# Kernel tuning notes

Measured on AMD Instinct MI355X. Metric: run time of the kernel, lower is better.

The kernel has to match this reference:

```python
import jax, jax.numpy as jnp
import numpy as np

C = 64
CQ = C // 8


def setup_inputs() -> dict:
    key = jax.random.key(0)
    ks = jax.random.split(key, 8)
    scale = 0.05
    x = jax.random.normal(ks[0], (4, C, 64, 64), dtype=jnp.float32)
    Wq = jax.random.normal(ks[1], (CQ, C), dtype=jnp.float32) * scale
    bq = jax.random.normal(ks[2], (CQ,), dtype=jnp.float32) * scale
    Wk = jax.random.normal(ks[3], (CQ, C), dtype=jnp.float32) * scale
    bk = jax.random.normal(ks[4], (CQ,), dtype=jnp.float32) * scale
    Wv = jax.random.normal(ks[5], (C, C), dtype=jnp.float32) * scale
    bv = jax.random.normal(ks[6], (C,), dtype=jnp.float32) * scale
    gamma = jnp.zeros((1,), dtype=jnp.float32) + 0.5  # nonzero so output depends on attention
    return {"x": x, "Wq": Wq, "bq": bq, "Wk": Wk, "bk": bk, "Wv": Wv, "bv": bv, "gamma": gamma}


def reference(x, Wq, bq, Wk, bk, Wv, bv, gamma):
    bs, c, h, w = x.shape
    hw = h * w
    xf = x.reshape(bs, c, hw)  # [b, c, hw]
    # 1x1 convs == per-pixel linear over channels
    Q = jnp.einsum('oc,bcn->bon', Wq, xf) + bq[None, :, None]  # [b, c/8, hw]
    K = jnp.einsum('oc,bcn->bon', Wk, xf) + bk[None, :, None]  # [b, c/8, hw]
    V = jnp.einsum('oc,bcn->bon', Wv, xf) + bv[None, :, None]  # [b, c, hw]
    # attention = softmax(Q^T K, axis=-1), NO scaling (matches source)
    scores = jnp.einsum('bqn,bqm->bnm', Q, K)  # [b, hw, hw]
    attn = jax.nn.softmax(scores, axis=-1)
    out = jnp.einsum('bcm,bmn->bcn', V, attn)  # torch.bmm(V_, attention)
    out = out.reshape(bs, c, h, w)
    return gamma[0] * out + x
```

## Files before the change

kernel.cpp:

```cpp
#include <hip/hip_runtime.h>


constexpr int Bn = 4, Cc = 64, Q8 = 8, Np = 4096;
constexpr int QK_STR = 32;
constexpr int PSTR = 40;
constexpr int NSL = 4;
constexpr int KSTR = 40;

typedef float f32x4 __attribute__((ext_vector_type(4)));
typedef short short8 __attribute__((ext_vector_type(8)));

__device__ inline unsigned int f2bf(float x) {
    unsigned int u = __float_as_uint(x);
    u += 0x7fff + ((u >> 16) & 1);
    return u >> 16;
}
__device__ inline float bf2f(unsigned int u) { return __uint_as_float(u << 16); }

__device__ inline unsigned cvt_pk_bf16(float a, float b) {
    unsigned r;
    asm("v_cvt_pk_bf16_f32 %0, %1, %2" : "=v"(r) : "v"(a), "v"(b));
    return r;
}
__device__ inline float exp2g(float x) {
#if __has_builtin(__builtin_amdgcn_exp2f)
    return __builtin_amdgcn_exp2f(x);
#else
    return exp2f(x);
#endif
}
__device__ inline float log2g(float x) {
#if __has_builtin(__builtin_amdgcn_logf)
    return __builtin_amdgcn_logf(x);
#else
    return log2f(x);
#endif
}

__global__ __launch_bounds__(64) void qkv_v2(
    const float* __restrict__ x,
    const float* __restrict__ Wq, const float* __restrict__ bq,
    const float* __restrict__ Wk, const float* __restrict__ bk,
    const float* __restrict__ Wv, const float* __restrict__ bv,
    unsigned short* __restrict__ Qp, unsigned short* __restrict__ Kp,
    unsigned short* __restrict__ Vb)
{
    const int lane = threadIdx.x;
    const int gpos = blockIdx.x * 64;
    const int os = blockIdx.y;
    const int b = gpos >> 12, n = (gpos & (Np - 1)) + lane;
    const float LOG2E = 1.4426950408889634f;

    float xv[Cc];
    const float* xp = x + (size_t)(b * Cc) * Np + n;
    #pragma unroll
    for (int c = 0; c < Cc; c++) xv[c] = xp[(size_t)c * Np];

    if (os == 0) {
        unsigned pk[4];
        float a0, a1;
        #pragma unroll
        for (int p = 0; p < 4; p++) {
            a0 = bq[2 * p]; a1 = bq[2 * p + 1];
            #pragma unroll
            for (int c = 0; c < Cc; c++) {
                a0 += Wq[(2 * p) * Cc + c] * xv[c];
                a1 += Wq[(2 * p + 1) * Cc + c] * xv[c];
            }
            pk[p] = f2bf(a0 * LOG2E) | (f2bf(a1 * LOG2E) << 16);
        }
        unsigned short* qrow = Qp + (size_t)(b * Np + n) * QK_STR;
        *(uint4*)qrow = make_uint4(pk[0], pk[1], pk[2], pk[3]);
        *(uint4*)(qrow + 8)  = make_uint4(0, 0, 0, 0);
        *(uint4*)(qrow + 16) = make_uint4(0, 0, 0, 0);
        *(uint4*)(qrow + 24) = make_uint4(0, 0, 0, 0);
        #pragma unroll
        for (int p = 0; p < 4; p++) {
            a0 = bk[2 * p]; a1 = bk[2 * p + 1];
            #pragma unroll
            for (int c = 0; c < Cc; c++) {
                a0 += Wk[(2 * p) * Cc + c] * xv[c];
                a1 += Wk[(2 * p + 1) * Cc + c] * xv[c];
            }
            pk[p] = f2bf(a0) | (f2bf(a1) << 16);
        }
        unsigned short* krow = Kp + (size_t)(b * Np + n) * QK_STR;
        *(uint4*)krow = make_uint4(pk[0], pk[1], pk[2], pk[3]);
        *(uint4*)(krow + 8)  = make_uint4(0, 0, 0, 0);
        *(uint4*)(krow + 16) = make_uint4(0, 0, 0, 0);
        *(uint4*)(krow + 24) = make_uint4(0, 0, 0, 0);
        #pragma unroll
        for (int o = 0; o < 4; o++) {
            float a = bv[o];
            #pragma unroll
            for (int c = 0; c < Cc; c++) a += Wv[o * Cc + c] * xv[c];
            Vb[(size_t)(b * Cc + o) * Np + n] = (unsigned short)f2bf(a);
        }
    } else {
        const int vbase = os * 20 - 16;
        #pragma unroll 4
        for (int o = 0; o < 20; o++) {
            const int vr = vbase + o;
            float a = bv[vr];
            #pragma unroll
            for (int c = 0; c < Cc; c++) a += Wv[vr * Cc + c] * xv[c];
            Vb[(size_t)(b * Cc + vr) * Np + n] = (unsigned short)f2bf(a);
        }
    }
}

__global__ __launch_bounds__(256) void zsum_v2(
    const unsigned short* __restrict__ Qp, const unsigned short* __restrict__ Kp,
    float* __restrict__ ZP)
{
    __shared__ unsigned short Klds[64 * KSTR];
    const int tid = threadIdx.x, w = tid >> 6, lane = tid & 63;
    const int quad = lane >> 4, l15 = lane & 15;
    const int bz = blockIdx.z, ns = blockIdx.y;
    const int m0 = blockIdx.x * 64 + w * 16;

    short8 qa = *(const short8*)&Qp[((size_t)(bz * Np + m0 + l15)) * QK_STR + quad * 8];

    const int rt = tid >> 2, ct = tid & 3;
    const int nbase = ns * (Np / NSL);
    const unsigned short* kbase = Kp + (size_t)bz * Np * QK_STR;

    uint4 pf = *(const uint4*)&kbase[(size_t)(nbase + rt) * QK_STR + ct * 8];
    float z0 = 0.f, z1 = 0.f, z2 = 0.f, z3 = 0.f;
    for (int nt = 0; nt < Np / NSL; nt += 64) {
        *(uint4*)&Klds[rt * KSTR + ct * 8] = pf;
        __syncthreads();
        if (nt + 64 < Np / NSL)
            pf = *(const uint4*)&kbase[(size_t)(nbase + nt + 64 + rt) * QK_STR + ct * 8];
        #pragma unroll
        for (int t16 = 0; t16 < 4; t16++) {
            short8 kb = *(const short8*)&Klds[(t16 * 16 + l15) * KSTR + quad * 8];
            f32x4 s = __builtin_amdgcn_mfma_f32_16x16x32_bf16(
                qa, kb, f32x4{0.f, 0.f, 0.f, 0.f}, 0, 0, 0);
            z0 += exp2g(s[0]); z1 += exp2g(s[1]);
            z2 += exp2g(s[2]); z3 += exp2g(s[3]);
        }
        __syncthreads();
    }
    #pragma unroll
    for (int mask = 1; mask < 16; mask <<= 1) {
        z0 += __shfl_xor(z0, mask); z1 += __shfl_xor(z1, mask);
        z2 += __shfl_xor(z2, mask); z3 += __shfl_xor(z3, mask);
    }
    if (l15 == 0) {
        float4 v = make_float4(z0, z1, z2, z3);
        *(float4*)&ZP[((size_t)(bz * NSL + ns)) * Np + m0 + quad * 4] = v;
    }
}

__global__ __launch_bounds__(256) void zred(
    const float* __restrict__ ZP, float* __restrict__ Lg)
{
    int i = blockIdx.x * 256 + threadIdx.x;
    int b = i >> 12, m = i & (Np - 1);
    float z = 0.f;
    #pragma unroll
    for (int s = 0; s < NSL; s++) z += ZP[((size_t)(b * NSL + s)) * Np + m];
    Lg[(size_t)b * Np + m] = -log2g(z);
}

__global__ __launch_bounds__(256) void attn_v4(
    const unsigned short* __restrict__ Qp, const unsigned short* __restrict__ Kp,
    const unsigned short* __restrict__ Vb, const float* __restrict__ Lg,
    unsigned short* __restrict__ PO, int Ms, int SL)
{
    __shared__ unsigned short Plds[128 * PSTR];
    const int tid = threadIdx.x, w = tid >> 6, lane = tid & 63;
    const int quad = lane >> 4, l15 = lane & 15;
    const int bz = blockIdx.z, by = blockIdx.y, nb = blockIdx.x * 128;

    short8 kf[2];
    #pragma unroll
    for (int t = 0; t < 2; t++) {
        int n = nb + (2 * w + t) * 16 + l15;
        kf[t] = *(const short8*)&Kp[((size_t)(bz * Np + n)) * QK_STR + quad * 8];
    }
    f32x4 acc[4][2];
    #pragma unroll
    for (int ct = 0; ct < 4; ct++)
        #pragma unroll
        for (int t = 0; t < 2; t++) acc[ct][t] = f32x4{0.f, 0.f, 0.f, 0.f};

    const int m_base = by * Ms;
    for (int mi = 0; mi < Ms; mi += 32) {
        const int m0 = m_base + mi;
        #pragma unroll
        for (int mt = 0; mt < 2; mt++) {
            short8 qa = *(const short8*)
                &Qp[((size_t)(bz * Np + m0 + mt * 16 + l15)) * QK_STR + quad * 8];
            f32x4 Lc = *(const f32x4*)
                &Lg[(size_t)bz * Np + m0 + mt * 16 + quad * 4];
            #pragma unroll
            for (int t = 0; t < 2; t++) {
                f32x4 s = __builtin_amdgcn_mfma_f32_16x16x32_bf16(qa, kf[t], Lc, 0, 0, 0);
                unsigned p01 = cvt_pk_bf16(exp2g(s[0]), exp2g(s[1]));
                unsigned p23 = cvt_pk_bf16(exp2g(s[2]), exp2g(s[3]));
                int nl = (2 * w + t) * 16 + l15;
                *(uint2*)&Plds[nl * PSTR + mt * 16 + quad * 4] = make_uint2(p01, p23);
            }
        }
        short8 pb[2];
        #pragma unroll
        for (int t = 0; t < 2; t++)
            pb[t] = *(const short8*)&Plds[(w * 32 + t * 16 + l15) * PSTR + quad * 8];
        #pragma unroll
        for (int ct = 0; ct < 4; ct++) {
            short8 ua = *(const short8*)
                &Vb[((size_t)(bz * Cc + ct * 16 + l15)) * Np + m0 + quad * 8];
            #pragma unroll
            for (int t = 0; t < 2; t++)
                acc[ct][t] = __builtin_amdgcn_mfma_f32_16x16x32_bf16(
                    ua, pb[t], acc[ct][t], 0, 0, 0);
        }
    }
    unsigned short* po = PO + ((size_t)((bz * SL + by) * Cc)) * Np + nb;
    #pragma unroll
    for (int ct = 0; ct < 4; ct++)
        #pragma unroll
        for (int t = 0; t < 2; t++) {
            int c = ct * 16 + quad * 4, n = w * 32 + t * 16 + l15;
            #pragma unroll
            for (int r = 0; r < 4; r++)
                po[(size_t)(c + r) * Np + n] = (unsigned short)f2bf(acc[ct][t][r]);
        }
}

__global__ __launch_bounds__(256) void combine_kernel(
    const unsigned short* __restrict__ PO, const float* __restrict__ x,
    const float* __restrict__ gamma, float* __restrict__ out, int sl2)
{
    int idx8 = (blockIdx.x * 256 + threadIdx.x) * 8;
    int b = idx8 >> 18;
    int c = (idx8 >> 12) & 63;
    int n = idx8 & (Np - 1);
    float o[8];
    #pragma unroll
    for (int i = 0; i < 8; i++) o[i] = 0.f;
    for (int sl = 0; sl < sl2; ++sl) {
        uint4 u = *(const uint4*)&PO[(size_t)((b * sl2 + sl) * Cc + c) * Np + n];
        o[0] += bf2f(u.x & 0xffff); o[1] += bf2f(u.x >> 16);
        o[2] += bf2f(u.y & 0xffff); o[3] += bf2f(u.y >> 16);
        o[4] += bf2f(u.z & 0xffff); o[5] += bf2f(u.z >> 16);
        o[6] += bf2f(u.w & 0xffff); o[7] += bf2f(u.w >> 16);
    }
    float g = gamma[0];
    float4 x0 = *(const float4*)&x[idx8];
    float4 x1 = *(const float4*)&x[idx8 + 4];
    float4 r0 = make_float4(g * o[0] + x0.x, g * o[1] + x0.y,
                            g * o[2] + x0.z, g * o[3] + x0.w);
    float4 r1 = make_float4(g * o[4] + x1.x, g * o[5] + x1.y,
                            g * o[6] + x1.z, g * o[7] + x1.w);
    *(float4*)&out[idx8] = r0;
    *(float4*)&out[idx8 + 4] = r1;
}

extern "C" void kernel_launch(void* const* d_in, const int* in_sizes, int n_in,
                              void* d_out, int out_size, void* d_ws, size_t ws_size,
                              hipStream_t stream)
{
    const float* x     = (const float*)d_in[0];
    const float* Wq    = (const float*)d_in[1];
    const float* bq    = (const float*)d_in[2];
    const float* Wk    = (const float*)d_in[3];
    const float* bk    = (const float*)d_in[4];
    const float* Wv    = (const float*)d_in[5];
    const float* bv    = (const float*)d_in[6];
    const float* gamma = (const float*)d_in[7];
    float* out = (float*)d_out;

    unsigned short* Qp = (unsigned short*)d_ws;
    unsigned short* Kp = Qp + (size_t)Bn * Np * QK_STR;
    unsigned short* Vb = Kp + (size_t)Bn * Np * QK_STR;
    float* Lg   = (float*)(Vb + (size_t)Bn * Cc * Np);
    float* ZP   = Lg + (size_t)Bn * Np;
    unsigned short* PO = (unsigned short*)(ZP + (size_t)Bn * NSL * Np);

    size_t baseB = (size_t)Bn * Np * QK_STR * 2 * 2 + (size_t)Bn * Cc * Np * 2
                 + (size_t)Bn * Np * 4 + (size_t)Bn * NSL * Np * 4;
    int SL = 4;
    while (SL > 1 && baseB + (size_t)Bn * SL * Cc * Np * 2 > ws_size) SL >>= 1;

    qkv_v2<<<dim3(Bn * Np / 64, 4), 64, 0, stream>>>(x, Wq, bq, Wk, bk, Wv, bv,
                                                     Qp, Kp, Vb);
    zsum_v2<<<dim3(Np / 64, NSL, Bn), 256, 0, stream>>>(Qp, Kp, ZP);
    zred<<<Bn * Np / 256, 256, 0, stream>>>(ZP, Lg);
    attn_v4<<<dim3(Np / 128, SL, Bn), 256, 0, stream>>>(Qp, Kp, Vb, Lg,
                                                        PO, Np / SL, SL);
    combine_kernel<<<Bn * Cc * Np / (256 * 8), 256, 0, stream>>>(PO, x, gamma, out, SL);
}
```

Measured before the change: 146.8 us.

## Split QKV projection wider, drop LDS staging in zsum, raise split counts

The QKV projection now launches 8 slices per pixel tile instead of 4: two slices compute Q and K separately, each with two V rows, and six slices compute 10 V rows each, which balances per-block work. The row-sum kernel stops staging K through shared memory with barriers and instead reads K fragments straight from global memory per MFMA tile, with the N range split 8 ways. The attention kernel's split count goes from 4 to 8, which adds parallelism but doubles the partial-output traffic the combine step has to read. Direct global loads rely on cache hits instead of LDS reuse.

Measured after the change: 147.2 us. Within noise of the previous version (+0.3%).

```diff
diff --git a/kernel.cpp b/kernel.cpp
--- a/kernel.cpp
+++ b/kernel.cpp
@@ -4,8 +4,7 @@
 constexpr int Bn = 4, Cc = 64, Q8 = 8, Np = 4096;
 constexpr int QK_STR = 32;
 constexpr int PSTR = 40;
-constexpr int NSL = 4;
-constexpr int KSTR = 40;
+constexpr int NSL = 8;
 
 typedef float f32x4 __attribute__((ext_vector_type(4)));
 typedef short short8 __attribute__((ext_vector_type(8)));
@@ -37,7 +36,7 @@
 #endif
 }
 
-__global__ __launch_bounds__(64) void qkv_v2(
+__global__ __launch_bounds__(64) void qkv_v3(
     const float* __restrict__ x,
     const float* __restrict__ Wq, const float* __restrict__ bq,
     const float* __restrict__ Wk, const float* __restrict__ bk,
@@ -56,91 +55,70 @@
     #pragma unroll
     for (int c = 0; c < Cc; c++) xv[c] = xp[(size_t)c * Np];
 
-    if (os == 0) {
+    if (os <= 1) {
+        const float* W = (os == 0) ? Wq : Wk;
+        const float* bb = (os == 0) ? bq : bk;
+        const float sc = (os == 0) ? LOG2E : 1.0f;
         unsigned pk[4];
-        float a0, a1;
         #pragma unroll
         for (int p = 0; p < 4; p++) {
-            a0 = bq[2 * p]; a1 = bq[2 * p + 1];
+            float a0 = bb[2 * p], a1 = bb[2 * p + 1];
             #pragma unroll
             for (int c = 0; c < Cc; c++) {
-                a0 += Wq[(2 * p) * Cc + c] * xv[c];
-                a1 += Wq[(2 * p + 1) * Cc + c] * xv[c];
+                a0 += W[(2 * p) * Cc + c] * xv[c];
+                a1 += W[(2 * p + 1) * Cc + c] * xv[c];
             }
-            pk[p] = f2bf(a0 * LOG2E) | (f2bf(a1 * LOG2E) << 16);
-        }
-        unsigned short* qrow = Qp + (size_t)(b * Np + n) * QK_STR;
-        *(uint4*)qrow = make_uint4(pk[0], pk[1], pk[2], pk[3]);
-        *(uint4*)(qrow + 8)  = make_uint4(0, 0, 0, 0);
-        *(uint4*)(qrow + 16) = make_uint4(0, 0, 0, 0);
-        *(uint4*)(qrow + 24) = make_uint4(0, 0, 0, 0);
-        #pragma unroll
-        for (int p = 0; p < 4; p++) {
-            a0 = bk[2 * p]; a1 = bk[2 * p + 1];
-            #pragma unroll
-            for (int c = 0; c < Cc; c++) {
-                a0 += Wk[(2 * p) * Cc + c] * xv[c];
-                a1 += Wk[(2 * p + 1) * Cc + c] * xv[c];
-            }
-            pk[p] = f2bf(a0) | (f2bf(a1) << 16);
-        }
-        unsigned short* krow = Kp + (size_t)(b * Np + n) * QK_STR;
-        *(uint4*)krow = make_uint4(pk[0], pk[1], pk[2], pk[3]);
-        *(uint4*)(krow + 8)  = make_uint4(0, 0, 0, 0);
-        *(uint4*)(krow + 16) = make_uint4(0, 0, 0, 0);
-        *(uint4*)(krow + 24) = make_uint4(0, 0, 0, 0);
-        #pragma unroll
-        for (int o = 0; o < 4; o++) {
-            float a = bv[o];
-            #pragma unroll
-            for (int c = 0; c < Cc; c++) a += Wv[o * Cc + c] * xv[c];
-            Vb[(size_t)(b * Cc + o) * Np + n] = (unsigned short)f2bf(a);
-        }
-    } else {
-        const int vbase = os * 20 - 16;
-        #pragma unroll 4
-        for (int o = 0; o < 20; o++) {
+            pk[p] = f2bf(a0 * sc) | (f2bf(a1 * sc) << 16);
+        }
+        unsigned short* row = (os == 0 ? Qp : Kp) + (size_t)(b * Np + n) * QK_STR;
+        *(uint4*)row = make_uint4(pk[0], pk[1], pk[2], pk[3]);
+        *(uint4*)(row + 8)  = make_uint4(0, 0, 0, 0);
+        *(uint4*)(row + 16) = make_uint4(0, 0, 0, 0);
+        *(uint4*)(row + 24) = make_uint4(0, 0, 0, 0);
+        const int vbase = 60 + (os == 0 ? 2 : 0);
+        #pragma unroll
+        for (int o = 0; o < 2; o++) {
             const int vr = vbase + o;
             float a = bv[vr];
             #pragma unroll
             for (int c = 0; c < Cc; c++) a += Wv[vr * Cc + c] * xv[c];
             Vb[(size_t)(b * Cc + vr) * Np + n] = (unsigned short)f2bf(a);
         }
-    }
-}
-
-__global__ __launch_bounds__(256) void zsum_v2(
+    } else {
+        const int vbase = (os - 2) * 10;
+        #pragma unroll
+        for (int o = 0; o < 10; o++) {
+            const int vr = vbase + o;
+            float a = bv[vr];
+            #pragma unroll
+            for (int c = 0; c < Cc; c++) a += Wv[vr * Cc + c] * xv[c];
+            Vb[(size_t)(b * Cc + vr) * Np + n] = (unsigned short)f2bf(a);
+        }
+    }
+}
+
+__global__ __launch_bounds__(256) void zsum_v3(
     const unsigned short* __restrict__ Qp, const unsigned short* __restrict__ Kp,
     float* __restrict__ ZP)
 {
-    __shared__ unsigned short Klds[64 * KSTR];
     const int tid = threadIdx.x, w = tid >> 6, lane = tid & 63;
     const int quad = lane >> 4, l15 = lane & 15;
     const int bz = blockIdx.z, ns = blockIdx.y;
     const int m0 = blockIdx.x * 64 + w * 16;
 
     short8 qa = *(const short8*)&Qp[((size_t)(bz * Np + m0 + l15)) * QK_STR + quad * 8];
-
-    const int rt = tid >> 2, ct = tid & 3;
+    const unsigned short* kbase = Kp + (size_t)bz * Np * QK_STR;
     const int nbase = ns * (Np / NSL);
-    const unsigned short* kbase = Kp + (size_t)bz * Np * QK_STR;
-
-    uint4 pf = *(const uint4*)&kbase[(size_t)(nbase + rt) * QK_STR + ct * 8];
+
     float z0 = 0.f, z1 = 0.f, z2 = 0.f, z3 = 0.f;
-    for (int nt = 0; nt < Np / NSL; nt += 64) {
-        *(uint4*)&Klds[rt * KSTR + ct * 8] = pf;
-        __syncthreads();
-        if (nt + 64 < Np / NSL)
-            pf = *(const uint4*)&kbase[(size_t)(nbase + nt + 64 + rt) * QK_STR + ct * 8];
-        #pragma unroll
-        for (int t16 = 0; t16 < 4; t16++) {
-            short8 kb = *(const short8*)&Klds[(t16 * 16 + l15) * KSTR + quad * 8];
-            f32x4 s = __builtin_amdgcn_mfma_f32_16x16x32_bf16(
-                qa, kb, f32x4{0.f, 0.f, 0.f, 0.f}, 0, 0, 0);
-            z0 += exp2g(s[0]); z1 += exp2g(s[1]);
-            z2 += exp2g(s[2]); z3 += exp2g(s[3]);
-        }
-        __syncthreads();
+    #pragma unroll 4
+    for (int nt = 0; nt < Np / NSL; nt += 16) {
+        short8 kb = *(const short8*)
+            &kbase[(size_t)(nbase + nt + l15) * QK_STR + quad * 8];
+        f32x4 s = __builtin_amdgcn_mfma_f32_16x16x32_bf16(
+            qa, kb, f32x4{0.f, 0.f, 0.f, 0.f}, 0, 0, 0);
+        z0 += exp2g(s[0]); z1 += exp2g(s[1]);
+        z2 += exp2g(s[2]); z3 += exp2g(s[3]);
     }
     #pragma unroll
     for (int mask = 1; mask < 16; mask <<= 1) {
@@ -282,12 +260,12 @@
 
     size_t baseB = (size_t)Bn * Np * QK_STR * 2 * 2 + (size_t)Bn * Cc * Np * 2
                  + (size_t)Bn * Np * 4 + (size_t)Bn * NSL * Np * 4;
-    int SL = 4;
+    int SL = 8;
     while (SL > 1 && baseB + (size_t)Bn * SL * Cc * Np * 2 > ws_size) SL >>= 1;
 
-    qkv_v2<<<dim3(Bn * Np / 64, 4), 64, 0, stream>>>(x, Wq, bq, Wk, bk, Wv, bv,
+    qkv_v3<<<dim3(Bn * Np / 64, 8), 64, 0, stream>>>(x, Wq, bq, Wk, bk, Wv, bv,
                                                      Qp, Kp, Vb);
-    zsum_v2<<<dim3(Np / 64, NSL, Bn), 256, 0, stream>>>(Qp, Kp, ZP);
+    zsum_v3<<<dim3(Np / 64, NSL, Bn), 256, 0, stream>>>(Qp, Kp, ZP);
     zred<<<Bn * Np / 256, 256, 0, stream>>>(ZP, Lg);
     attn_v4<<<dim3(Np / 128, SL, Bn), 256, 0, stream>>>(Qp, Kp, Vb, Lg,
                                                         PO, Np / SL, SL);
```
